# Optimization experiments

Measured on AMD Instinct MI355X. Metric: run time of the kernel, lower is better.

## Reference

```python
import jax, jax.numpy as jnp
import numpy as np

DIMS = 2048
HEADS = 16
HEAD_DIM = DIMS // HEADS  # 128
WIN = 256
THETA = 10000.0


def rotate_half(x):
    x1, x2 = jnp.split(x, 2, axis=-1)
    return jnp.concatenate([-x2, x1], axis=-1)


def rope_freqs(seq_len):
    inv_freq = 1.0 / (THETA ** (jnp.arange(0, HEAD_DIM, 2, dtype=jnp.float32) / HEAD_DIM))
    f = jnp.outer(jnp.arange(seq_len, dtype=jnp.float32), inv_freq)  # [S, D/2]
    return jnp.concatenate([f, f], axis=-1)[None, :, None, :]  # [1, S, 1, D]


def setup_inputs() -> dict:
    key = jax.random.key(0)
    ks = jax.random.split(key, 5)
    B, S = 2, 8192
    scale = 1.0 / np.sqrt(DIMS).astype(np.float32)
    return {
        "hidden_states": jax.random.normal(ks[0], (B, S, DIMS), jnp.float32),
        "Wq": jax.random.normal(ks[1], (DIMS, DIMS), jnp.float32) * scale,
        "Wk": jax.random.normal(ks[2], (DIMS, DIMS), jnp.float32) * scale,
        "Wv": jax.random.normal(ks[3], (DIMS, DIMS), jnp.float32) * scale,
        "Wo": jax.random.normal(ks[4], (DIMS, DIMS), jnp.float32) * scale,
    }


def reference(hidden_states, Wq, Wk, Wv, Wo):
    B, S, _ = hidden_states.shape
    # projections (weights stored [in, out])
    q = (hidden_states @ Wq).reshape(B, S, HEADS, HEAD_DIM)
    k = (hidden_states @ Wk).reshape(B, S, HEADS, HEAD_DIM)
    v = (hidden_states @ Wv).reshape(B, S, HEADS, HEAD_DIM)

    freqs = rope_freqs(S)
    cos, sin = jnp.cos(freqs), jnp.sin(freqs)
    q = q * cos + rotate_half(q) * sin
    k = k * cos + rotate_half(k) * sin

    C = S // WIN
    qc = q.reshape(B, C, WIN, HEADS, HEAD_DIM)
    kc = k.reshape(B, C, WIN, HEADS, HEAD_DIM)
    vc = v.reshape(B, C, WIN, HEADS, HEAD_DIM)

    # previous chunk's K/V (zeros for chunk 0; masked out anyway)
    kp = jnp.concatenate([jnp.zeros_like(kc[:, :1]), kc[:, :-1]], axis=1)
    vp = jnp.concatenate([jnp.zeros_like(vc[:, :1]), vc[:, :-1]], axis=1)
    kcat = jnp.concatenate([kp, kc], axis=2)  # [B, C, 2W, H, D]
    vcat = jnp.concatenate([vp, vc], axis=2)

    scores = jnp.einsum('bcqhd,bckhd->bchqk', qc, kcat) / np.float32(np.sqrt(HEAD_DIM))

    causal = jnp.tril(jnp.ones((WIN, WIN), dtype=bool))  # current-chunk causal
    prev_ok = (jnp.arange(C) > 0)[:, None, None]  # chunk 0 has no previous chunk
    mask = jnp.concatenate([
        jnp.broadcast_to(prev_ok, (C, WIN, WIN)),
        jnp.broadcast_to(causal[None], (C, WIN, WIN)),
    ], axis=-1)  # [C, W, 2W]

    scores = jnp.where(mask[None, :, None], scores, -jnp.inf)
    probs = jax.nn.softmax(scores, axis=-1)
    out = jnp.einsum('bchqk,bckhd->bcqhd', probs, vcat)
    out = out.reshape(B, S, DIMS)
    return out @ Wo
```

## Files before the change

### kernel.cpp

```cpp
#include <hip/hip_runtime.h>
#include <cmath>

#define DIMS 2048
#define SEQ  8192
#define NB   2
#define HEADS 16
#define HD   128
#define WINW 256
#define MROWS 16384
#define NCH  32

using bf16x8 = __attribute__((ext_vector_type(8))) short;
using f32x4  = __attribute__((ext_vector_type(4))) float;

__device__ __forceinline__ unsigned short f2bf(float f) {
  unsigned int u = __float_as_uint(f);
  u += 0x7FFF + ((u >> 16) & 1);
  return (unsigned short)(u >> 16);
}

__device__ __forceinline__ void async16(const unsigned short* g, unsigned short* l) {
  __builtin_amdgcn_global_load_lds((const __attribute__((address_space(1))) void*)g,
                                   (__attribute__((address_space(3))) void*)l,
                                   16, 0, 0);
}

#define BAR() __builtin_amdgcn_s_barrier()
#define WAIT_LGKM0() do { asm volatile("s_waitcnt lgkmcnt(0)" ::: "memory"); \
                          __builtin_amdgcn_sched_barrier(0); } while (0)
#define WAIT_VM(n) asm volatile("s_waitcnt vmcnt(" #n ")" ::: "memory")
#define MFMA16(a, b, c) __builtin_amdgcn_mfma_f32_16x16x32_bf16(a, b, c, 0, 0, 0)

__global__ void wconv(const float* __restrict__ w0, const float* __restrict__ w1,
                      const float* __restrict__ w2, const float* __restrict__ w3,
                      unsigned short* __restrict__ Wt) {
  __shared__ unsigned short tile[64][65];
  const float* W = (blockIdx.z == 0) ? w0 : (blockIdx.z == 1) ? w1 : (blockIdx.z == 2) ? w2 : w3;
  unsigned short* O = Wt + (size_t)blockIdx.z * DIMS * DIMS;
  const int k0 = blockIdx.y * 64, n0 = blockIdx.x * 64;
  const int t = threadIdx.x;
  #pragma unroll
  for (int p = 0; p < 16; ++p) {
    int i = p * 4 + (t >> 6);
    int j = t & 63;
    tile[i][j] = f2bf(W[(size_t)(k0 + i) * DIMS + n0 + j]);
  }
  __syncthreads();
  #pragma unroll
  for (int p = 0; p < 16; ++p) {
    int a = p * 4 + (t >> 6);
    int b = t & 63;
    O[(size_t)(n0 + a) * DIMS + k0 + b] = tile[b][a];
  }
}

__global__ void hconv(const float* __restrict__ in, unsigned short* __restrict__ outp) {
  const long n4 = (long)MROWS * DIMS / 4;
  long i = (long)blockIdx.x * blockDim.x + threadIdx.x;
  const long stride = (long)gridDim.x * blockDim.x;
  for (; i < n4; i += stride) {
    float4 v = ((const float4*)in)[i];
    ushort4 o;
    o.x = f2bf(v.x); o.y = f2bf(v.y); o.z = f2bf(v.z); o.w = f2bf(v.w);
    ((ushort4*)outp)[i] = o;
  }
}

__global__ void rope_tab(float* __restrict__ cosT, float* __restrict__ sinT) {
  int t = blockIdx.x * 256 + threadIdx.x;
  int pos = t >> 6, i = t & 63;
  double inv = pow(10000.0, -(double)i / 64.0);
  double ang = (double)pos * inv;
  cosT[t] = (float)cos(ang);
  sinT[t] = (float)sin(ang);
}

template<int MODE>
__global__ __launch_bounds__(512, 2) void gemm256(
    const unsigned short* __restrict__ A,
    const unsigned short* __restrict__ WtAll,
    unsigned short* __restrict__ OutB,
    float* __restrict__ OutF,
    const float* __restrict__ cosT,
    const float* __restrict__ sinT) {
  __shared__ __align__(1024) unsigned short lds[65536];
  unsigned short* const As0 = lds;
  unsigned short* const Bs0 = lds + 16384;
  unsigned short* const As1 = lds + 32768;
  unsigned short* const Bs1 = lds + 49152;

  const int tid = threadIdx.x;
  const int wid = tid >> 6, lane = tid & 63;
  const int lo = lane & 15, hi = lane >> 4;
  const int wm = wid >> 2, wn = wid & 3;
  const int flip = (lo & 7) << 4;

  const int nwg = gridDim.x;
  const int orig = blockIdx.x;
  const int bid = (orig & 7) * (nwg >> 3) + (orig >> 3);

  const int z = (MODE == 0) ? (bid >> 9) : 3;
  const int by = (MODE == 0) ? ((bid & 511) >> 3) : (bid >> 3);
  const int bx = bid & 7;
  const int m0 = by * 256, n0 = bx * 256;
  const unsigned short* const Ag = A;
  const unsigned short* const Bg = WtAll + (size_t)z * DIMS * DIMS;

  f32x4 acc[8][4];
  #pragma unroll
  for (int i = 0; i < 8; ++i)
    #pragma unroll
    for (int j = 0; j < 4; ++j)
      acc[i][j] = (f32x4){0.f, 0.f, 0.f, 0.f};

  auto stage_half = [&](const unsigned short* __restrict__ G, int grow0, int tile,
                        unsigned short* dst) {
    const int k0 = tile * 64;
    #pragma unroll
    for (int h8 = 0; h8 < 2; ++h8) {
      const int c = h8 * 8 + wid;
      const int row = c * 8 + (lane >> 3);
      const int col8 = (lane & 7) ^ (lane >> 3);
      async16(G + (size_t)(grow0 + row) * DIMS + k0 + col8 * 8, dst + c * 512);
    }
  };
  auto rdA = [&](const unsigned short* base, int i, int kk) -> bf16x8 {
    const int r = i * 32 + wm * 16 + lo;
    const int cb = (kk * 64 + hi * 16) ^ flip;
    return *(const bf16x8*)((const char*)base + r * 128 + cb);
  };
  auto rdB = [&](const unsigned short* base, int j, int kk) -> bf16x8 {
    const int r = j * 64 + wn * 16 + lo;
    const int cb = (kk * 64 + hi * 16) ^ flip;
    return *(const bf16x8*)((const char*)base + r * 128 + cb);
  };

  bf16x8 aq[4][2], b0[2][2], b1[2][2];

  stage_half(Ag, m0,       0, As0);
  stage_half(Bg, n0,       0, Bs0);
  stage_half(Ag, m0 + 128, 0, As0 + 8192);
  stage_half(Bg, n0 + 128, 0, Bs0 + 8192);
  stage_half(Ag, m0,       1, As1);
  stage_half(Bg, n0,       1, Bs1);
  stage_half(Bg, n0 + 128, 1, Bs1 + 8192);
  WAIT_VM(6);
  BAR();

  #pragma unroll 1
  for (int it = 0; it < 16; ++it) {
    const int t = 2 * it;
    const bool pre = (it < 15);
    #pragma unroll
    for (int i = 0; i < 4; ++i) { aq[i][0] = rdA(As0, i, 0); aq[i][1] = rdA(As0, i, 1); }
    #pragma unroll
    for (int j = 0; j < 2; ++j) { b0[j][0] = rdB(Bs0, j, 0); b0[j][1] = rdB(Bs0, j, 1); }
    stage_half(Ag, m0 + 128, t + 1, As1 + 8192);
    BAR(); WAIT_LGKM0();
    __builtin_amdgcn_s_setprio(1);
    #pragma unroll
    for (int kk = 0; kk < 2; ++kk)
      #pragma unroll
      for (int i = 0; i < 4; ++i)
        #pragma unroll
        for (int j = 0; j < 2; ++j)
          acc[i][j] = MFMA16(aq[i][kk], b0[j][kk], acc[i][j]);
    __builtin_amdgcn_s_setprio(0);
    BAR();
    #pragma unroll
    for (int j = 0; j < 2; ++j) { b1[j][0] = rdB(Bs0, 2 + j, 0); b1[j][1] = rdB(Bs0, 2 + j, 1); }
    if (pre) stage_half(Ag, m0, t + 2, As0);
    BAR(); WAIT_LGKM0();
    __builtin_amdgcn_s_setprio(1);
    #pragma unroll
    for (int kk = 0; kk < 2; ++kk)
      #pragma unroll
      for (int i = 0; i < 4; ++i)
        #pragma unroll
        for (int j = 0; j < 2; ++j)
          acc[i][2 + j] = MFMA16(aq[i][kk], b1[j][kk], acc[i][2 + j]);
    __builtin_amdgcn_s_setprio(0);
    BAR();
    #pragma unroll
    for (int i = 0; i < 4; ++i) { aq[i][0] = rdA(As0, 4 + i, 0); aq[i][1] = rdA(As0, 4 + i, 1); }
    if (pre) stage_half(Bg, n0, t + 2, Bs0);
    BAR(); WAIT_LGKM0();
    __builtin_amdgcn_s_setprio(1);
    #pragma unroll
    for (int kk = 0; kk < 2; ++kk)
      #pragma unroll
      for (int i = 0; i < 4; ++i)
        #pragma unroll
        for (int j = 0; j < 2; ++j)
          acc[4 + i][j] = MFMA16(aq[i][kk], b0[j][kk], acc[4 + i][j]);
    __builtin_amdgcn_s_setprio(0);
    BAR();
    if (pre) stage_half(Bg, n0 + 128, t + 2, Bs0 + 8192);
    BAR();
    __builtin_amdgcn_s_setprio(1);
    #pragma unroll
    for (int kk = 0; kk < 2; ++kk)
      #pragma unroll
      for (int i = 0; i < 4; ++i)
        #pragma unroll
        for (int j = 0; j < 2; ++j)
          acc[4 + i][2 + j] = MFMA16(aq[i][kk], b1[j][kk], acc[4 + i][2 + j]);
    __builtin_amdgcn_s_setprio(0);
    if (it == 15) { WAIT_VM(0); } else { WAIT_VM(6); }
    BAR();
    #pragma unroll
    for (int i = 0; i < 4; ++i) { aq[i][0] = rdA(As1, i, 0); aq[i][1] = rdA(As1, i, 1); }
    #pragma unroll
    for (int j = 0; j < 2; ++j) { b0[j][0] = rdB(Bs1, j, 0); b0[j][1] = rdB(Bs1, j, 1); }
    if (pre) stage_half(Ag, m0 + 128, t + 2, As0 + 8192);
    BAR(); WAIT_LGKM0();
    __builtin_amdgcn_s_setprio(1);
    #pragma unroll
    for (int kk = 0; kk < 2; ++kk)
      #pragma unroll
      for (int i = 0; i < 4; ++i)
        #pragma unroll
        for (int j = 0; j < 2; ++j)
          acc[i][j] = MFMA16(aq[i][kk], b0[j][kk], acc[i][j]);
    __builtin_amdgcn_s_setprio(0);
    BAR();
    #pragma unroll
    for (int j = 0; j < 2; ++j) { b1[j][0] = rdB(Bs1, 2 + j, 0); b1[j][1] = rdB(Bs1, 2 + j, 1); }
    if (pre) stage_half(Ag, m0, t + 3, As1);
    BAR(); WAIT_LGKM0();
    __builtin_amdgcn_s_setprio(1);
    #pragma unroll
    for (int kk = 0; kk < 2; ++kk)
      #pragma unroll
      for (int i = 0; i < 4; ++i)
        #pragma unroll
        for (int j = 0; j < 2; ++j)
          acc[i][2 + j] = MFMA16(aq[i][kk], b1[j][kk], acc[i][2 + j]);
    __builtin_amdgcn_s_setprio(0);
    BAR();
    #pragma unroll
    for (int i = 0; i < 4; ++i) { aq[i][0] = rdA(As1, 4 + i, 0); aq[i][1] = rdA(As1, 4 + i, 1); }
    if (pre) stage_half(Bg, n0, t + 3, Bs1);
    BAR(); WAIT_LGKM0();
    __builtin_amdgcn_s_setprio(1);
    #pragma unroll
    for (int kk = 0; kk < 2; ++kk)
      #pragma unroll
      for (int i = 0; i < 4; ++i)
        #pragma unroll
        for (int j = 0; j < 2; ++j)
          acc[4 + i][j] = MFMA16(aq[i][kk], b0[j][kk], acc[4 + i][j]);
    __builtin_amdgcn_s_setprio(0);
    BAR();
    if (pre) stage_half(Bg, n0 + 128, t + 3, Bs1 + 8192);
    BAR();
    __builtin_amdgcn_s_setprio(1);
    #pragma unroll
    for (int kk = 0; kk < 2; ++kk)
      #pragma unroll
      for (int i = 0; i < 4; ++i)
        #pragma unroll
        for (int j = 0; j < 2; ++j)
          acc[4 + i][2 + j] = MFMA16(aq[i][kk], b1[j][kk], acc[4 + i][2 + j]);
    __builtin_amdgcn_s_setprio(0);
    WAIT_VM(6);
    BAR();
  }

  const int rope = (MODE == 0) && (z < 2);
  unsigned short* outb = (MODE == 0) ? (OutB + (size_t)z * MROWS * DIMS) : (unsigned short*)nullptr;
  #pragma unroll
  for (int i = 0; i < 8; ++i) {
    #pragma unroll
    for (int rr = 0; rr < 4; ++rr) {
      const int row = m0 + i * 32 + wm * 16 + hi * 4 + rr;
      const int s = row & (SEQ - 1);
      if (MODE == 1) {
        float* o = OutF + (size_t)row * DIMS + n0;
        #pragma unroll
        for (int j = 0; j < 4; ++j) o[j * 64 + wn * 16 + lo] = acc[i][j][rr];
      } else if (rope) {
        unsigned short* o = outb + (size_t)row * DIMS + n0;
        const int d = wn * 16 + lo;
        const float c = cosT[s * 64 + d], sn = sinT[s * 64 + d];
        #pragma unroll
        for (int p = 0; p < 2; ++p) {
          const float v1 = acc[i][2 * p][rr], v2 = acc[i][2 * p + 1][rr];
          o[p * 128 + d]      = f2bf(v1 * c - v2 * sn);
          o[p * 128 + d + 64] = f2bf(v2 * c + v1 * sn);
        }
      } else {
        unsigned short* o = outb + (size_t)row * DIMS + n0;
        #pragma unroll
        for (int j = 0; j < 4; ++j) o[j * 64 + wn * 16 + lo] = f2bf(acc[i][j][rr]);
      }
    }
  }
}

__global__ __launch_bounds__(512) void attn(
    const unsigned short* __restrict__ Qb,
    const unsigned short* __restrict__ Kb,
    const unsigned short* __restrict__ Vb,
    unsigned short* __restrict__ AO) {
  __shared__ unsigned short Ksm[64 * 136];
  __shared__ unsigned short Vsm[128 * 72];
  __shared__ unsigned short Psm[8 * 32 * 72];

  const int bid = blockIdx.x;
  const int h = bid & 15;
  const int c = (bid >> 4) & 31;
  const int b = bid >> 9;
  const int tid = threadIdx.x;
  const int wid = tid >> 6, lane = tid & 63;
  const int lo = lane & 15, hi = lane >> 4;
  const float SCALE = 0.08838834764831845f;

  bf16x8 qf[2][4];
  {
    const size_t base = ((size_t)(b * SEQ + c * WINW + wid * 32 + lo)) * DIMS + h * HD;
    #pragma unroll
    for (int m = 0; m < 2; ++m)
      #pragma unroll
      for (int ks = 0; ks < 4; ++ks)
        qf[m][ks] = *(const bf16x8*)&Qb[base + (size_t)m * 16 * DIMS + ks * 32 + hi * 8];
  }

  f32x4 O[2][8];
  float mrow[2][4], lrow[2][4];
  #pragma unroll
  for (int m = 0; m < 2; ++m) {
    #pragma unroll
    for (int n = 0; n < 8; ++n) O[m][n] = (f32x4){0.f, 0.f, 0.f, 0.f};
    #pragma unroll
    for (int r = 0; r < 4; ++r) { mrow[m][r] = -INFINITY; lrow[m][r] = 0.f; }
  }

  unsigned short* Pw = Psm + wid * 32 * 72;
  const int t0 = (c == 0) ? 4 : 0;

  for (int t = t0; t < 8; ++t) {
    const int krow_base = b * SEQ + (c - 1) * WINW + t * 64;
    #pragma unroll
    for (int i = 0; i < 2; ++i) {
      const int cid = i * 512 + tid;
      const int kr = cid >> 4;
      const int d8 = (cid & 15) << 3;
      *(bf16x8*)&Ksm[kr * 136 + d8] =
          *(const bf16x8*)&Kb[(size_t)(krow_base + kr) * DIMS + h * HD + d8];
      bf16x8 v = *(const bf16x8*)&Vb[(size_t)(krow_base + kr) * DIMS + h * HD + d8];
      #pragma unroll
      for (int e = 0; e < 8; ++e)
        Vsm[(d8 + e) * 72 + kr] = (unsigned short)v[e];
    }
    __syncthreads();

    f32x4 S[2][4];
    #pragma unroll
    for (int m = 0; m < 2; ++m)
      #pragma unroll
      for (int n = 0; n < 4; ++n)
        S[m][n] = (f32x4){0.f, 0.f, 0.f, 0.f};
    #pragma unroll
    for (int ks = 0; ks < 4; ++ks) {
      const int ko = ks * 32 + hi * 8;
      bf16x8 kf[4];
      #pragma unroll
      for (int n = 0; n < 4; ++n)
        kf[n] = *(const bf16x8*)&Ksm[(n * 16 + lo) * 136 + ko];
      #pragma unroll
      for (int m = 0; m < 2; ++m)
        #pragma unroll
        for (int n = 0; n < 4; ++n)
          S[m][n] = __builtin_amdgcn_mfma_f32_16x16x32_bf16(qf[m][ks], kf[n], S[m][n], 0, 0, 0);
    }

    #pragma unroll
    for (int m = 0; m < 2; ++m) {
      #pragma unroll
      for (int r = 0; r < 4; ++r) {
        const int qrow = wid * 32 + m * 16 + hi * 4 + r;
        float tmax = -INFINITY;
        #pragma unroll
        for (int n = 0; n < 4; ++n) {
          const int kc = t * 64 + n * 16 + lo;
          float v = S[m][n][r] * SCALE;
          const bool ok = (kc < WINW) ? (c > 0) : ((kc - WINW) <= qrow);
          v = ok ? v : -INFINITY;
          S[m][n][r] = v;
          tmax = fmaxf(tmax, v);
        }
        tmax = fmaxf(tmax, __shfl_xor(tmax, 1));
        tmax = fmaxf(tmax, __shfl_xor(tmax, 2));
        tmax = fmaxf(tmax, __shfl_xor(tmax, 4));
        tmax = fmaxf(tmax, __shfl_xor(tmax, 8));
        const float mold = mrow[m][r];
        const float mnew = fmaxf(mold, tmax);
        const float corr = __expf(mold - mnew);
        float rsum = 0.f;
        #pragma unroll
        for (int n = 0; n < 4; ++n) {
          const float p = __expf(S[m][n][r] - mnew);
          S[m][n][r] = p;
          rsum += p;
        }
        rsum += __shfl_xor(rsum, 1);
        rsum += __shfl_xor(rsum, 2);
        rsum += __shfl_xor(rsum, 4);
        rsum += __shfl_xor(rsum, 8);
        mrow[m][r] = mnew;
        lrow[m][r] = lrow[m][r] * corr + rsum;
        #pragma unroll
        for (int n = 0; n < 8; ++n) O[m][n][r] *= corr;
        #pragma unroll
        for (int n = 0; n < 4; ++n)
          Pw[(m * 16 + hi * 4 + r) * 72 + n * 16 + lo] = f2bf(S[m][n][r]);
      }
    }
    asm volatile("" ::: "memory");

    #pragma unroll
    for (int kk = 0; kk < 2; ++kk) {
      const int ko = kk * 32 + hi * 8;
      bf16x8 pf[2], vf[8];
      #pragma unroll
      for (int m = 0; m < 2; ++m)
        pf[m] = *(const bf16x8*)&Pw[(m * 16 + lo) * 72 + ko];
      #pragma unroll
      for (int n = 0; n < 8; ++n)
        vf[n] = *(const bf16x8*)&Vsm[(n * 16 + lo) * 72 + ko];
      #pragma unroll
      for (int m = 0; m < 2; ++m)
        #pragma unroll
        for (int n = 0; n < 8; ++n)
          O[m][n] = __builtin_amdgcn_mfma_f32_16x16x32_bf16(pf[m], vf[n], O[m][n], 0, 0, 0);
    }
    __syncthreads();
  }

  #pragma unroll
  for (int m = 0; m < 2; ++m) {
    #pragma unroll
    for (int r = 0; r < 4; ++r) {
      const float inv = 1.f / lrow[m][r];
      const size_t row = (size_t)(b * SEQ + c * WINW + wid * 32 + m * 16 + hi * 4 + r);
      unsigned short* o = AO + row * DIMS + h * HD;
      #pragma unroll
      for (int n = 0; n < 8; ++n)
        o[n * 16 + lo] = f2bf(O[m][n][r] * inv);
    }
  }
}

extern "C" void kernel_launch(void* const* d_in, const int* in_sizes, int n_in,
                              void* d_out, int out_size, void* d_ws, size_t ws_size,
                              hipStream_t stream) {
  const float* H  = (const float*)d_in[0];
  const float* Wq = (const float*)d_in[1];
  const float* Wk = (const float*)d_in[2];
  const float* Wv = (const float*)d_in[3];
  const float* Wo = (const float*)d_in[4];
  float* out = (float*)d_out;

  unsigned short* Wt  = (unsigned short*)d_ws;
  unsigned short* Hb  = Wt + (size_t)4 * DIMS * DIMS;
  unsigned short* QKV = Hb + (size_t)MROWS * DIMS;
  unsigned short* AO  = QKV + (size_t)3 * MROWS * DIMS;
  float* cosT = (float*)(AO + (size_t)MROWS * DIMS);
  float* sinT = cosT + (size_t)SEQ * 64;

  wconv<<<dim3(32, 32, 4), 256, 0, stream>>>(Wq, Wk, Wv, Wo, Wt);
  hconv<<<2048, 256, 0, stream>>>(H, Hb);
  rope_tab<<<2048, 256, 0, stream>>>(cosT, sinT);
  gemm256<0><<<1536, 512, 0, stream>>>(Hb, Wt, QKV, nullptr, cosT, sinT);
  attn<<<dim3(1024), 512, 0, stream>>>(QKV, QKV + (size_t)MROWS * DIMS,
                                       QKV + (size_t)2 * MROWS * DIMS, AO);
  gemm256<1><<<512, 512, 0, stream>>>(AO, Wt, nullptr, out, cosT, sinT);
}
```

Measured before the change: 817.0 us.

## Write V transposed from projection, double-buffer async K/V loads, lazy softmax rescale

The QKV projection epilogue now writes V transposed (per batch, feature-major over sequence), and the grid mapping interleaves the three projections per row block. The attention kernel stages K and V^T with async global-to-LDS loads into double buffers using an XOR swizzle, so the next tile's load overlaps compute and the per-element transpose scatter into LDS goes away. Softmax skips rescaling O and l when the running max does not grow by more than a threshold, saving multiplies at the cost of a slightly larger exponent range. The transposed V stores are narrow strided writes, which may make that epilogue more expensive.

```diff
diff --git a/kernel.cpp b/kernel.cpp
--- a/kernel.cpp
+++ b/kernel.cpp
@@ -99,9 +99,15 @@
   const int orig = blockIdx.x;
   const int bid = (orig & 7) * (nwg >> 3) + (orig >> 3);
 
-  const int z = (MODE == 0) ? (bid >> 9) : 3;
-  const int by = (MODE == 0) ? ((bid & 511) >> 3) : (bid >> 3);
-  const int bx = bid & 7;
+  int by, bx, z;
+  if (MODE == 0) {
+    by = bid / 24;
+    const int rem = bid - by * 24;
+    z = rem >> 3;
+    bx = rem & 7;
+  } else {
+    by = bid >> 3; bx = bid & 7; z = 3;
+  }
   const int m0 = by * 256, n0 = bx * 256;
   const unsigned short* const Ag = A;
   const unsigned short* const Bg = WtAll + (size_t)z * DIMS * DIMS;
@@ -267,32 +273,46 @@
     BAR();
   }
 
-  const int rope = (MODE == 0) && (z < 2);
-  unsigned short* outb = (MODE == 0) ? (OutB + (size_t)z * MROWS * DIMS) : (unsigned short*)nullptr;
-  #pragma unroll
-  for (int i = 0; i < 8; ++i) {
-    #pragma unroll
-    for (int rr = 0; rr < 4; ++rr) {
-      const int row = m0 + i * 32 + wm * 16 + hi * 4 + rr;
-      const int s = row & (SEQ - 1);
-      if (MODE == 1) {
-        float* o = OutF + (size_t)row * DIMS + n0;
-        #pragma unroll
-        for (int j = 0; j < 4; ++j) o[j * 64 + wn * 16 + lo] = acc[i][j][rr];
-      } else if (rope) {
-        unsigned short* o = outb + (size_t)row * DIMS + n0;
-        const int d = wn * 16 + lo;
-        const float c = cosT[s * 64 + d], sn = sinT[s * 64 + d];
-        #pragma unroll
-        for (int p = 0; p < 2; ++p) {
-          const float v1 = acc[i][2 * p][rr], v2 = acc[i][2 * p + 1][rr];
-          o[p * 128 + d]      = f2bf(v1 * c - v2 * sn);
-          o[p * 128 + d + 64] = f2bf(v2 * c + v1 * sn);
+  if (MODE == 0 && z == 2) {
+    unsigned short* vt = OutB + (size_t)2 * MROWS * DIMS;
+    #pragma unroll
+    for (int i = 0; i < 8; ++i) {
+      const int row0 = m0 + i * 32 + wm * 16 + hi * 4;
+      const int bb = row0 >> 13;
+      const int s0 = row0 & (SEQ - 1);
+      #pragma unroll
+      for (int j = 0; j < 4; ++j) {
+        const int colg = n0 + j * 64 + wn * 16 + lo;
+        ushort4 pk;
+        pk.x = f2bf(acc[i][j][0]); pk.y = f2bf(acc[i][j][1]);
+        pk.z = f2bf(acc[i][j][2]); pk.w = f2bf(acc[i][j][3]);
+        *(ushort4*)&vt[(((size_t)(bb * 2048 + colg)) << 13) + s0] = pk;
+      }
+    }
+  } else {
+    unsigned short* outb = (MODE == 0) ? (OutB + (size_t)z * MROWS * DIMS)
+                                       : (unsigned short*)nullptr;
+    #pragma unroll
+    for (int i = 0; i < 8; ++i) {
+      #pragma unroll
+      for (int rr = 0; rr < 4; ++rr) {
+        const int row = m0 + i * 32 + wm * 16 + hi * 4 + rr;
+        const int s = row & (SEQ - 1);
+        if (MODE == 1) {
+          float* o = OutF + (size_t)row * DIMS + n0;
+          #pragma unroll
+          for (int j = 0; j < 4; ++j) o[j * 64 + wn * 16 + lo] = acc[i][j][rr];
+        } else {
+          unsigned short* o = outb + (size_t)row * DIMS + n0;
+          const int d = wn * 16 + lo;
+          const float cc = cosT[s * 64 + d], sn = sinT[s * 64 + d];
+          #pragma unroll
+          for (int p = 0; p < 2; ++p) {
+            const float v1 = acc[i][2 * p][rr], v2 = acc[i][2 * p + 1][rr];
+            o[p * 128 + d]      = f2bf(v1 * cc - v2 * sn);
+            o[p * 128 + d + 64] = f2bf(v2 * cc + v1 * sn);
+          }
         }
-      } else {
-        unsigned short* o = outb + (size_t)row * DIMS + n0;
-        #pragma unroll
-        for (int j = 0; j < 4; ++j) o[j * 64 + wn * 16 + lo] = f2bf(acc[i][j][rr]);
       }
     }
   }
@@ -301,10 +321,10 @@
 __global__ __launch_bounds__(512) void attn(
     const unsigned short* __restrict__ Qb,
     const unsigned short* __restrict__ Kb,
-    const unsigned short* __restrict__ Vb,
+    const unsigned short* __restrict__ Vt,
     unsigned short* __restrict__ AO) {
-  __shared__ unsigned short Ksm[64 * 136];
-  __shared__ unsigned short Vsm[128 * 72];
+  __shared__ unsigned short Ksm[2][64 * 128];
+  __shared__ unsigned short Vsm[2][128 * 64];
   __shared__ unsigned short Psm[8 * 32 * 72];
 
   const int bid = blockIdx.x;
@@ -339,21 +359,31 @@
   unsigned short* Pw = Psm + wid * 32 * 72;
   const int t0 = (c == 0) ? 4 : 0;
 
+  const unsigned short* Kg0 = Kb + ((size_t)(b * SEQ + (c - 1) * WINW)) * DIMS + h * HD;
+  const unsigned short* Vg0 = Vt + (((size_t)(b * 2048 + h * HD)) << 13) + (c - 1) * WINW;
+
+  auto stageKV = [&](int t, int pb) {
+    #pragma unroll
+    for (int p = 0; p < 2; ++p) {
+      const int cid = p * 512 + tid;
+      const int row = cid >> 4, c16 = cid & 15;
+      async16(Kg0 + (size_t)(t * 64 + row) * DIMS + ((c16 ^ (row & 7)) << 3),
+              &Ksm[pb][cid * 8]);
+    }
+    #pragma unroll
+    for (int p = 0; p < 2; ++p) {
+      const int cid = p * 512 + tid;
+      const int rd = cid >> 3, c8 = cid & 7;
+      async16(Vg0 + ((size_t)rd << 13) + t * 64 + ((c8 ^ (rd & 7)) << 3),
+              &Vsm[pb][cid * 8]);
+    }
+  };
+
+  stageKV(t0, t0 & 1);
   for (int t = t0; t < 8; ++t) {
-    const int krow_base = b * SEQ + (c - 1) * WINW + t * 64;
-    #pragma unroll
-    for (int i = 0; i < 2; ++i) {
-      const int cid = i * 512 + tid;
-      const int kr = cid >> 4;
-      const int d8 = (cid & 15) << 3;
-      *(bf16x8*)&Ksm[kr * 136 + d8] =
-          *(const bf16x8*)&Kb[(size_t)(krow_base + kr) * DIMS + h * HD + d8];
-      bf16x8 v = *(const bf16x8*)&Vb[(size_t)(krow_base + kr) * DIMS + h * HD + d8];
-      #pragma unroll
-      for (int e = 0; e < 8; ++e)
-        Vsm[(d8 + e) * 72 + kr] = (unsigned short)v[e];
-    }
-    __syncthreads();
+    const int pb = t & 1;
+    if (t < 7) { stageKV(t + 1, pb ^ 1); WAIT_VM(4); } else { WAIT_VM(0); }
+    BAR();
 
     f32x4 S[2][4];
     #pragma unroll
@@ -361,26 +391,28 @@
       #pragma unroll
       for (int n = 0; n < 4; ++n)
         S[m][n] = (f32x4){0.f, 0.f, 0.f, 0.f};
+    const char* Kbase = (const char*)&Ksm[pb][0];
     #pragma unroll
     for (int ks = 0; ks < 4; ++ks) {
-      const int ko = ks * 32 + hi * 8;
       bf16x8 kf[4];
       #pragma unroll
       for (int n = 0; n < 4; ++n)
-        kf[n] = *(const bf16x8*)&Ksm[(n * 16 + lo) * 136 + ko];
+        kf[n] = *(const bf16x8*)(Kbase + (n * 16 + lo) * 256 +
+                                 (((ks * 4 + hi) ^ (lo & 7)) << 4));
       #pragma unroll
       for (int m = 0; m < 2; ++m)
         #pragma unroll
         for (int n = 0; n < 4; ++n)
-          S[m][n] = __builtin_amdgcn_mfma_f32_16x16x32_bf16(qf[m][ks], kf[n], S[m][n], 0, 0, 0);
-    }
-
+          S[m][n] = MFMA16(qf[m][ks], kf[n], S[m][n]);
+    }
+
+    float tmax[2][4];
     #pragma unroll
     for (int m = 0; m < 2; ++m) {
       #pragma unroll
       for (int r = 0; r < 4; ++r) {
         const int qrow = wid * 32 + m * 16 + hi * 4 + r;
-        float tmax = -INFINITY;
+        float tm = -INFINITY;
         #pragma unroll
         for (int n = 0; n < 4; ++n) {
           const int kc = t * 64 + n * 16 + lo;
@@ -388,19 +420,40 @@
           const bool ok = (kc < WINW) ? (c > 0) : ((kc - WINW) <= qrow);
           v = ok ? v : -INFINITY;
           S[m][n][r] = v;
-          tmax = fmaxf(tmax, v);
+          tm = fmaxf(tm, v);
         }
-        tmax = fmaxf(tmax, __shfl_xor(tmax, 1));
-        tmax = fmaxf(tmax, __shfl_xor(tmax, 2));
-        tmax = fmaxf(tmax, __shfl_xor(tmax, 4));
-        tmax = fmaxf(tmax, __shfl_xor(tmax, 8));
-        const float mold = mrow[m][r];
-        const float mnew = fmaxf(mold, tmax);
-        const float corr = __expf(mold - mnew);
+        tm = fmaxf(tm, __shfl_xor(tm, 1));
+        tm = fmaxf(tm, __shfl_xor(tm, 2));
+        tm = fmaxf(tm, __shfl_xor(tm, 4));
+        tm = fmaxf(tm, __shfl_xor(tm, 8));
+        tmax[m][r] = tm;
+      }
+    }
+    float need = -INFINITY;
+    #pragma unroll
+    for (int m = 0; m < 2; ++m)
+      #pragma unroll
+      for (int r = 0; r < 4; ++r)
+        need = fmaxf(need, tmax[m][r] - mrow[m][r]);
+    const bool fast = __all(need <= 8.0f);
+
+    #pragma unroll
+    for (int m = 0; m < 2; ++m) {
+      #pragma unroll
+      for (int r = 0; r < 4; ++r) {
+        float mused = mrow[m][r];
+        if (!fast) {
+          mused = fmaxf(mused, tmax[m][r]);
+          const float corr = __expf(mrow[m][r] - mused);
+          lrow[m][r] *= corr;
+          #pragma unroll
+          for (int n = 0; n < 8; ++n) O[m][n][r] *= corr;
+          mrow[m][r] = mused;
+        }
         float rsum = 0.f;
         #pragma unroll
         for (int n = 0; n < 4; ++n) {
-          const float p = __expf(S[m][n][r] - mnew);
+          const float p = __expf(S[m][n][r] - mused);
           S[m][n][r] = p;
           rsum += p;
         }
@@ -408,10 +461,7 @@
         rsum += __shfl_xor(rsum, 2);
         rsum += __shfl_xor(rsum, 4);
         rsum += __shfl_xor(rsum, 8);
-        mrow[m][r] = mnew;
-        lrow[m][r] = lrow[m][r] * corr + rsum;
-        #pragma unroll
-        for (int n = 0; n < 8; ++n) O[m][n][r] *= corr;
+        lrow[m][r] += rsum;
         #pragma unroll
         for (int n = 0; n < 4; ++n)
           Pw[(m * 16 + hi * 4 + r) * 72 + n * 16 + lo] = f2bf(S[m][n][r]);
@@ -419,6 +469,7 @@
     }
     asm volatile("" ::: "memory");
 
+    const char* Vbase = (const char*)&Vsm[pb][0];
     #pragma unroll
     for (int kk = 0; kk < 2; ++kk) {
       const int ko = kk * 32 + hi * 8;
@@ -428,14 +479,15 @@
         pf[m] = *(const bf16x8*)&Pw[(m * 16 + lo) * 72 + ko];
       #pragma unroll
       for (int n = 0; n < 8; ++n)
-        vf[n] = *(const bf16x8*)&Vsm[(n * 16 + lo) * 72 + ko];
+        vf[n] = *(const bf16x8*)(Vbase + (n * 16 + lo) * 128 +
+                                 (((kk * 4 + hi) ^ (lo & 7)) << 4));
       #pragma unroll
       for (int m = 0; m < 2; ++m)
         #pragma unroll
         for (int n = 0; n < 8; ++n)
-          O[m][n] = __builtin_amdgcn_mfma_f32_16x16x32_bf16(pf[m], vf[n], O[m][n], 0, 0, 0);
-    }
-    __syncthreads();
+          O[m][n] = MFMA16(pf[m], vf[n], O[m][n]);
+    }
+    BAR();
   }
 
   #pragma unroll
```

After: 739.6 us. 9.5% less time.
